# Optimization experiments

Measured on AMD Instinct MI355X. Metric: run time of the kernel, lower is better.

Reference implementation:

```python
import jax, jax.numpy as jnp
import numpy as np

DIM = 2048
N_HEADS = 32
N_KV_HEADS = 8
HEAD_DIM = DIM // N_HEADS  # 64
N_REP = N_HEADS // N_KV_HEADS  # 4
B, S = 1, 2048


def _rope(t, cos, sin):
    # t: (b, s, h, head_dim); cos/sin: (s, head_dim//2)
    tr = t.reshape(*t.shape[:-1], -1, 2)
    a, b = tr[..., 0], tr[..., 1]
    c = cos[None, :, None, :]
    s_ = sin[None, :, None, :]
    ra = a * c - b * s_
    rb = a * s_ + b * c
    return jnp.stack([ra, rb], axis=-1).reshape(t.shape)


def setup_inputs() -> dict:
    key = jax.random.key(0)
    ks = jax.random.split(key, 6)
    sc = 1.0 / np.sqrt(DIM)
    x = jax.random.normal(ks[0], (B, S, DIM), dtype=jnp.float32)
    wq = jax.random.normal(ks[1], (DIM, N_HEADS * HEAD_DIM), dtype=jnp.float32) * sc
    wk = jax.random.normal(ks[2], (DIM, N_KV_HEADS * HEAD_DIM), dtype=jnp.float32) * sc
    wv = jax.random.normal(ks[3], (DIM, N_KV_HEADS * HEAD_DIM), dtype=jnp.float32) * sc
    wo = jax.random.normal(ks[4], (N_HEADS * HEAD_DIM, DIM), dtype=jnp.float32) * sc
    # rotary frequencies (theta = 500000 as in Llama3)
    inv = 1.0 / (500000.0 ** (np.arange(0, HEAD_DIM, 2, dtype=np.float32) / HEAD_DIM))
    ang = np.arange(S, dtype=np.float32)[:, None] * inv[None, :]
    freqs_cos = jnp.asarray(np.cos(ang), dtype=jnp.float32)
    freqs_sin = jnp.asarray(np.sin(ang), dtype=jnp.float32)
    # causal additive mask
    mask = jnp.triu(jnp.full((S, S), -1e9, dtype=jnp.float32), k=1)
    return {"x": x, "wq": wq, "wk": wk, "wv": wv, "wo": wo,
            "freqs_cos": freqs_cos, "freqs_sin": freqs_sin, "mask": mask,
            "start_pos": 0}


def reference(x, wq, wk, wv, wo, freqs_cos, freqs_sin, mask, start_pos):
    b, s, _ = x.shape
    xq = (x @ wq).reshape(b, s, N_HEADS, HEAD_DIM)
    xk = (x @ wk).reshape(b, s, N_KV_HEADS, HEAD_DIM)
    xv = (x @ wv).reshape(b, s, N_KV_HEADS, HEAD_DIM)
    xq = _rope(xq, freqs_cos, freqs_sin)
    xk = _rope(xk, freqs_cos, freqs_sin)
    # GQA without repeat_interleave: view queries as (b, s, kv, rep, d)
    q = xq.reshape(b, s, N_KV_HEADS, N_REP, HEAD_DIM)
    scale = 1.0 / np.sqrt(HEAD_DIM)
    # scores: (b, kv, rep, q, k)
    scores = jnp.einsum('bqkrd,bskd->bkrqs', q, xk) * scale
    scores = scores + mask[None, None, None, :, :]
    probs = jax.nn.softmax(scores.astype(jnp.float32), axis=-1).astype(x.dtype)
    out = jnp.einsum('bkrqs,bskd->bqkrd', probs, xv)
    out = out.reshape(b, s, N_HEADS * HEAD_DIM)
    return out @ wo
```

## Files before the change

kernel.cpp:

```cpp
#include <hip/hip_runtime.h>
#include <hip/hip_bf16.h>

#define DIM 2048
#define S_LEN 2048
#define N_HEADS 32
#define N_KV_HEADS 8
#define HEAD_DIM 64
#define KV_DIM (N_KV_HEADS * HEAD_DIM)
#define QKV_N (DIM + 2 * KV_DIM)
#define QSCALE 0.18033688011112042f

typedef __attribute__((ext_vector_type(8))) short bf16x8;
typedef __attribute__((ext_vector_type(4))) float f32x4;

__device__ __forceinline__ unsigned short bf16_of(float f) {
    __hip_bfloat16 h = __float2bfloat16(f);
    return *reinterpret_cast<unsigned short*>(&h);
}
__device__ __forceinline__ float f_of_bf16(unsigned short u) {
    unsigned int x = ((unsigned int)u) << 16;
    return __uint_as_float(x);
}
__device__ __forceinline__ void gl_lds16(const void* g, void* l) {
    __builtin_amdgcn_global_load_lds((const __attribute__((address_space(1))) void*)g,
                                     (__attribute__((address_space(3))) void*)l, 16, 0, 0);
}
__device__ __forceinline__ unsigned int pack2tr(float lo, float hi) {
    return __builtin_amdgcn_perm(__float_as_uint(hi), __float_as_uint(lo), 0x07060302u);
}

__global__ __launch_bounds__(256) void prep(const float* __restrict__ x,
                                            const float* __restrict__ wq,
                                            const float* __restrict__ wk,
                                            const float* __restrict__ wv,
                                            const float* __restrict__ wo,
                                            unsigned short* __restrict__ xbf,
                                            unsigned short* __restrict__ wqkvT,
                                            unsigned short* __restrict__ woT) {
    __shared__ float tile[64][65];
    const int t = threadIdx.x;
    int b = blockIdx.x;
    if (b < 4096) {
        int idx = b * 256 + t;
        float4 f = ((const float4*)x)[idx];
        ushort4 u;
        u.x = bf16_of(f.x); u.y = bf16_of(f.y); u.z = bf16_of(f.z); u.w = bf16_of(f.w);
        ((ushort4*)xbf)[idx] = u;
        return;
    }
    b -= 4096;
    const float* src;
    unsigned short* dst;
    int src_cols, bx, by;
    if (b < 1024)      { src = wq; dst = wqkvT;                                src_cols = DIM;    bx = b & 31;          by = b >> 5; }
    else if (b < 1280) { src = wk; dst = wqkvT + (size_t)DIM * DIM;            src_cols = KV_DIM; bx = (b - 1024) & 7;  by = (b - 1024) >> 3; }
    else if (b < 1536) { src = wv; dst = wqkvT + (size_t)(DIM + KV_DIM) * DIM; src_cols = KV_DIM; bx = (b - 1280) & 7;  by = (b - 1280) >> 3; }
    else               { src = wo; dst = woT;                                  src_cols = DIM;    bx = (b - 1536) & 31; by = (b - 1536) >> 5; }
    const int c0 = bx * 64, r0 = by * 64;
#pragma unroll
    for (int i = 0; i < 16; i++) {
        int idx = t + i * 256;
        int r = idx >> 6, c = idx & 63;
        tile[r][c] = src[(size_t)(r0 + r) * src_cols + c0 + c];
    }
    __syncthreads();
#pragma unroll
    for (int i = 0; i < 16; i++) {
        int idx = t + i * 256;
        int r = idx >> 6, c = idx & 63;
        dst[(size_t)(c0 + r) * DIM + r0 + c] = bf16_of(tile[c][r]);
    }
}

__global__ __launch_bounds__(256) void gemm_bt64(const unsigned short* __restrict__ A,
                                                 const unsigned short* __restrict__ Bt,
                                                 void* __restrict__ Cv,
                                                 int M, int N, int K, int c_bf16) {
    __shared__ unsigned short As[128 * 64];
    __shared__ unsigned short Bs[64 * 64];
    const int tid = threadIdx.x;
    const int wave = tid >> 6, lane = tid & 63;
    const int m16 = lane & 15, quad = lane >> 4;
    const int m0 = blockIdx.y * 128, n0 = blockIdx.x * 64;
    const int wm = (wave >> 1) * 64, wn = (wave & 1) * 32;

    const int lrow = lane >> 3;
    const int gc = (lane & 7) ^ lrow;
    const unsigned short* Ab = A + (size_t)(m0 + wave * 8 + lrow) * K + gc * 8;
    const unsigned short* Bb = Bt + (size_t)(n0 + wave * 8 + lrow) * K + gc * 8;

    f32x4 acc[4][2];
#pragma unroll
    for (int mb = 0; mb < 4; mb++)
#pragma unroll
        for (int nb = 0; nb < 2; nb++) acc[mb][nb] = (f32x4){0.f, 0.f, 0.f, 0.f};

    for (int k0 = 0; k0 < K; k0 += 64) {
#pragma unroll
        for (int g = 0; g < 4; g++)
            gl_lds16(Ab + (size_t)g * 32 * K + k0, &As[(g * 32 + wave * 8) * 64]);
#pragma unroll
        for (int g = 0; g < 2; g++)
            gl_lds16(Bb + (size_t)g * 32 * K + k0, &Bs[(g * 32 + wave * 8) * 64]);
        __syncthreads();
#pragma unroll
        for (int ks = 0; ks < 2; ks++) {
            const int ch = (ks * 4 + quad) ^ (m16 & 7);
            bf16x8 af[4], bfr[2];
#pragma unroll
            for (int mb = 0; mb < 4; mb++)
                af[mb] = *(const bf16x8*)&As[(wm + mb * 16 + m16) * 64 + ch * 8];
#pragma unroll
            for (int nb = 0; nb < 2; nb++)
                bfr[nb] = *(const bf16x8*)&Bs[(wn + nb * 16 + m16) * 64 + ch * 8];
#pragma unroll
            for (int mb = 0; mb < 4; mb++)
#pragma unroll
                for (int nb = 0; nb < 2; nb++)
                    acc[mb][nb] = __builtin_amdgcn_mfma_f32_16x16x32_bf16(af[mb], bfr[nb], acc[mb][nb], 0, 0, 0);
        }
        __syncthreads();
    }

    if (c_bf16) {
        unsigned short* C = (unsigned short*)Cv;
#pragma unroll
        for (int mb = 0; mb < 4; mb++)
#pragma unroll
            for (int nb = 0; nb < 2; nb++)
#pragma unroll
                for (int r = 0; r < 4; r++)
                    C[(size_t)(m0 + wm + mb * 16 + quad * 4 + r) * N + n0 + wn + nb * 16 + m16] =
                        bf16_of(acc[mb][nb][r]);
    } else {
        float* C = (float*)Cv;
#pragma unroll
        for (int mb = 0; mb < 4; mb++)
#pragma unroll
            for (int nb = 0; nb < 2; nb++)
#pragma unroll
                for (int r = 0; r < 4; r++)
                    C[(size_t)(m0 + wm + mb * 16 + quad * 4 + r) * N + n0 + wn + nb * 16 + m16] =
                        acc[mb][nb][r];
    }
}

__global__ __launch_bounds__(256) void rope_tv(const unsigned short* __restrict__ qkv,
                                               unsigned short* __restrict__ qbf,
                                               unsigned short* __restrict__ kbf,
                                               unsigned short* __restrict__ vbt,
                                               const float* __restrict__ fcos,
                                               const float* __restrict__ fsin) {
    __shared__ unsigned short tile[64][65];
    const int t = threadIdx.x;
    int b = blockIdx.x;
    if (b < 2560) {
        int idx = b * 256 + t;
        const int nq = S_LEN * N_HEADS * 8;
        int s, j, srcoff, dstoff;
        unsigned short* dst;
        float osc;
        if (idx < nq) {
            s = idx >> 8;
            int rem = idx & 255;
            int h = rem >> 3;
            j = rem & 7;
            srcoff = s * QKV_N + h * 64 + j * 8;
            dstoff = s * DIM + h * 64 + j * 8;
            dst = qbf;
            osc = QSCALE;
        } else {
            int t2 = idx - nq;
            s = t2 >> 6;
            int rem = t2 & 63;
            int h = rem >> 3;
            j = rem & 7;
            srcoff = s * QKV_N + DIM + h * 64 + j * 8;
            dstoff = s * KV_DIM + h * 64 + j * 8;
            dst = kbf;
            osc = 1.0f;
        }
        bf16x8 v8 = *(const bf16x8*)&qkv[srcoff];
        float4 c4 = *(const float4*)&fcos[s * 32 + j * 4];
        float4 s4 = *(const float4*)&fsin[s * 32 + j * 4];
        float cs[4] = {c4.x, c4.y, c4.z, c4.w};
        float sn[4] = {s4.x, s4.y, s4.z, s4.w};
        bf16x8 o;
#pragma unroll
        for (int p = 0; p < 4; p++) {
            float a = f_of_bf16((unsigned short)v8[2 * p]);
            float bb = f_of_bf16((unsigned short)v8[2 * p + 1]);
            o[2 * p]     = (short)bf16_of((a * cs[p] - bb * sn[p]) * osc);
            o[2 * p + 1] = (short)bf16_of((a * sn[p] + bb * cs[p]) * osc);
        }
        *(bf16x8*)&dst[dstoff] = o;
        return;
    }
    b -= 2560;
    const int d0 = (b & 7) * 64;
    const int s0 = (b >> 3) * 64;
#pragma unroll
    for (int i = 0; i < 16; i++) {
        int idx = t + i * 256;
        int r = idx >> 6, c = idx & 63;
        tile[r][c] = qkv[(size_t)(s0 + r) * QKV_N + DIM + KV_DIM + d0 + c];
    }
    __syncthreads();
#pragma unroll
    for (int i = 0; i < 16; i++) {
        int idx = t + i * 256;
        int r = idx >> 6, c = idx & 63;
        int key = s0 + c;
        int kl = key & 127;
        int kp = (kl & 0x60) | ((kl & 0x0C) << 1) | ((kl & 0x10) >> 2) | (kl & 3);
        vbt[(size_t)(d0 + r) * S_LEN + (key & ~127) + kp] = tile[c][r];
    }
}

__global__ __launch_bounds__(256) void attn_mfma5(const unsigned short* __restrict__ qb,
                                                  const unsigned short* __restrict__ kb,
                                                  const unsigned short* __restrict__ vbt,
                                                  unsigned short* __restrict__ out) {
    const int h  = blockIdx.y;
    const int bx = blockIdx.x;
    const int kh = h >> 2;
    const int tid  = threadIdx.x;
    const int wave = tid >> 6;
    const int lane = tid & 63;
    const int m16  = lane & 15;
    const int quad = lane >> 4;

    __shared__ unsigned short Ks[2][128 * 64];
    __shared__ unsigned short Vt[2][64 * 128];

    const int lrow8 = lane >> 3;
    const int kc    = (lane & 7) ^ lrow8;
    const int lrow4 = lane >> 4;
    const int vc    = (lane & 15) ^ ((wave * 4 + lrow4) & 7);

    const unsigned short* Kbase = kb + (size_t)kh * 64 + (size_t)(wave * 8 + lrow8) * KV_DIM + kc * 8;
    const unsigned short* Vbase = vbt + (size_t)(kh * 64 + wave * 4 + lrow4) * S_LEN + vc * 8;

    bf16x8 ones;
#pragma unroll
    for (int i = 0; i < 8; i++) ones[i] = (short)0x3F80;

#pragma unroll
    for (int half = 0; half < 2; half++) {
        const int qt = half ? bx : (31 - bx);
        const int q0 = qt * 64;
        const int n_iter = (qt >> 1) + 1;

        bf16x8 qa[2];
        {
            const int qrow = q0 + wave * 16 + m16;
#pragma unroll
            for (int ks = 0; ks < 2; ks++)
                qa[ks] = *(const bf16x8*)&qb[(size_t)qrow * DIM + h * 64 + ks * 32 + quad * 8];
        }

        f32x4 o_acc[4];
#pragma unroll
        for (int nb = 0; nb < 4; nb++) o_acc[nb] = (f32x4){0.f, 0.f, 0.f, 0.f};
        f32x4 l_acc = (f32x4){0.f, 0.f, 0.f, 0.f};
        float m_s = -1e30f;
        const int qrow_lane = q0 + wave * 16 + m16;
        const int orow_base = q0 + wave * 16 + quad * 4;

        if (half) __syncthreads();

#pragma unroll
        for (int g = 0; g < 4; g++) {
            gl_lds16(Kbase + (size_t)(g * 32) * KV_DIM, &Ks[0][(g * 32 + wave * 8) * 64]);
            gl_lds16(Vbase + (size_t)g * 16 * S_LEN, &Vt[0][(g * 16 + wave * 4) * 128]);
        }

        for (int kt = 0; kt < n_iter; kt++) {
            __syncthreads();
            if (kt + 1 < n_iter) {
                const int nb2 = (kt + 1) & 1;
#pragma unroll
                for (int g = 0; g < 4; g++) {
                    gl_lds16(Kbase + (size_t)((kt + 1) * 128 + g * 32) * KV_DIM,
                             &Ks[nb2][(g * 32 + wave * 8) * 64]);
                    gl_lds16(Vbase + (size_t)g * 16 * S_LEN + (kt + 1) * 128,
                             &Vt[nb2][(g * 16 + wave * 4) * 128]);
                }
            }
            const unsigned short* K_ = Ks[kt & 1];
            const unsigned short* V_ = Vt[kt & 1];

            f32x4 sc[8];
#pragma unroll
            for (int cb = 0; cb < 8; cb++) sc[cb] = (f32x4){0.f, 0.f, 0.f, 0.f};
#pragma unroll
            for (int ks = 0; ks < 2; ks++) {
                const int slot = (ks * 4 + quad) ^ (m16 & 7);
#pragma unroll
                for (int cb = 0; cb < 8; cb++) {
                    bf16x8 kf = *(const bf16x8*)&K_[(cb * 16 + m16) * 64 + slot * 8];
                    sc[cb] = __builtin_amdgcn_mfma_f32_16x16x32_bf16(kf, qa[ks], sc[cb], 0, 0, 0);
                }
            }

            if (kt == n_iter - 1) {
#pragma unroll
                for (int cb = 0; cb < 8; cb++) {
                    int key = kt * 128 + cb * 16 + quad * 4;
#pragma unroll
                    for (int r = 0; r < 4; r++)
                        if (key + r > qrow_lane) sc[cb][r] = -1e30f;
                }
            }

            float rmax = fmaxf(fmaxf(sc[0][0], sc[0][1]), fmaxf(sc[0][2], sc[0][3]));
#pragma unroll
            for (int cb = 1; cb < 8; cb++) {
                float c1 = fmaxf(fmaxf(sc[cb][0], sc[cb][1]), fmaxf(sc[cb][2], sc[cb][3]));
                rmax = fmaxf(rmax, c1);
            }
            rmax = fmaxf(rmax, __shfl_xor(rmax, 16, 64));
            rmax = fmaxf(rmax, __shfl_xor(rmax, 32, 64));

            float mnew = fmaxf(m_s, rmax);
            float alpha = __builtin_amdgcn_exp2f(m_s - mnew);
            m_s = mnew;

#pragma unroll
            for (int cb = 0; cb < 8; cb++)
#pragma unroll
                for (int r = 0; r < 4; r++)
                    sc[cb][r] = __builtin_amdgcn_exp2f(sc[cb][r] - mnew);

            unsigned int P01[8], P23[8];
#pragma unroll
            for (int cb = 0; cb < 8; cb++) {
                P01[cb] = pack2tr(sc[cb][0], sc[cb][1]);
                P23[cb] = pack2tr(sc[cb][2], sc[cb][3]);
            }

#pragma unroll
            for (int r = 0; r < 4; r++) {
                float a_r = __shfl(alpha, quad * 4 + r, 64);
#pragma unroll
                for (int nb = 0; nb < 4; nb++) o_acc[nb][r] *= a_r;
                l_acc[r] *= a_r;
            }

#pragma unroll
            for (int ks = 0; ks < 4; ks++) {
                union { unsigned int u[4]; bf16x8 v; } pa;
                pa.u[0] = P01[2 * ks];     pa.u[1] = P23[2 * ks];
                pa.u[2] = P01[2 * ks + 1]; pa.u[3] = P23[2 * ks + 1];
                const int slot = (ks * 4 + quad) ^ (m16 & 7);
#pragma unroll
                for (int nb = 0; nb < 4; nb++) {
                    bf16x8 vf = *(const bf16x8*)&V_[(nb * 16 + m16) * 128 + slot * 8];
                    o_acc[nb] = __builtin_amdgcn_mfma_f32_16x16x32_bf16(pa.v, vf, o_acc[nb], 0, 0, 0);
                }
                l_acc = __builtin_amdgcn_mfma_f32_16x16x32_bf16(pa.v, ones, l_acc, 0, 0, 0);
            }
        }

#pragma unroll
        for (int r = 0; r < 4; r++) {
            float inv_l = 1.f / l_acc[r];
#pragma unroll
            for (int nb = 0; nb < 4; nb++)
                out[(size_t)(orow_base + r) * DIM + h * 64 + nb * 16 + m16] =
                    bf16_of(o_acc[nb][r] * inv_l);
        }
    }
}

extern "C" void kernel_launch(void* const* d_in, const int* in_sizes, int n_in,
                              void* d_out, int out_size, void* d_ws, size_t ws_size,
                              hipStream_t stream) {
    const float* x    = (const float*)d_in[0];
    const float* wq   = (const float*)d_in[1];
    const float* wk   = (const float*)d_in[2];
    const float* wv   = (const float*)d_in[3];
    const float* wo   = (const float*)d_in[4];
    const float* fcos = (const float*)d_in[5];
    const float* fsin = (const float*)d_in[6];

    char* ws = (char*)d_ws;
    const size_t MB = 1024 * 1024;
    unsigned short* xbf    = (unsigned short*)(ws);
    unsigned short* wqkvT  = (unsigned short*)(ws + 8 * MB);
    unsigned short* woT    = (unsigned short*)(ws + 20 * MB);
    unsigned short* qkvbf  = (unsigned short*)(ws + 28 * MB);
    unsigned short* vbt    = (unsigned short*)(ws + 40 * MB);
    unsigned short* qbf    = (unsigned short*)(ws + 8 * MB);
    unsigned short* kbf    = (unsigned short*)(ws + 16 * MB);
    unsigned short* attnbf = (unsigned short*)(ws);

    prep<<<4096 + 2560, 256, 0, stream>>>(x, wq, wk, wv, wo, xbf, wqkvT, woT);

    gemm_bt64<<<dim3(QKV_N / 64, S_LEN / 128), 256, 0, stream>>>(xbf, wqkvT, qkvbf,
                                                                 S_LEN, QKV_N, DIM, 1);

    rope_tv<<<2560 + 256, 256, 0, stream>>>(qkvbf, qbf, kbf, vbt, fcos, fsin);

    attn_mfma5<<<dim3(16, N_HEADS), 256, 0, stream>>>(qbf, kbf, vbt, attnbf);

    gemm_bt64<<<dim3(DIM / 64, S_LEN / 128), 256, 0, stream>>>(attnbf, woT, d_out,
                                                               S_LEN, DIM, DIM, 0);
}
```

Measured before the change: 227.7 us.

## Process 128-row query tiles per block, sharing K/V loads across two sub-tiles

The attention kernel no longer processes two balanced 64-row query tiles one after the other. Each block now handles one 128-row query tile, and each wave keeps two 16-row sub-tiles (A and B) in registers. Every K fragment and V fragment read from LDS feeds two MFMAs, which halves K/V global-to-LDS traffic per query row and doubles the independent MFMA chains. In exchange, register use goes up and the old pairing that balanced causal work across blocks is gone. The new code relies on launching heavy tiles first to keep per-block work even.

Measured after the change: 242.4 us. +6.5%, slower.

```diff
diff --git a/kernel.cpp b/kernel.cpp
--- a/kernel.cpp
+++ b/kernel.cpp
@@ -217,12 +217,14 @@
     }
 }
 
-__global__ __launch_bounds__(256) void attn_mfma5(const unsigned short* __restrict__ qb,
+__global__ __launch_bounds__(256) void attn_mfma6(const unsigned short* __restrict__ qb,
                                                   const unsigned short* __restrict__ kb,
                                                   const unsigned short* __restrict__ vbt,
                                                   unsigned short* __restrict__ out) {
     const int h  = blockIdx.y;
-    const int bx = blockIdx.x;
+    const int qt = 15 - blockIdx.x;
+    const int q0 = qt * 128;
+    const int n_iter = qt + 1;
     const int kh = h >> 2;
     const int tid  = threadIdx.x;
     const int wave = tid >> 6;
@@ -245,130 +247,143 @@
 #pragma unroll
     for (int i = 0; i < 8; i++) ones[i] = (short)0x3F80;
 
-#pragma unroll
-    for (int half = 0; half < 2; half++) {
-        const int qt = half ? bx : (31 - bx);
-        const int q0 = qt * 64;
-        const int n_iter = (qt >> 1) + 1;
-
-        bf16x8 qa[2];
-        {
-            const int qrow = q0 + wave * 16 + m16;
-#pragma unroll
-            for (int ks = 0; ks < 2; ks++)
-                qa[ks] = *(const bf16x8*)&qb[(size_t)qrow * DIM + h * 64 + ks * 32 + quad * 8];
-        }
-
-        f32x4 o_acc[4];
-#pragma unroll
-        for (int nb = 0; nb < 4; nb++) o_acc[nb] = (f32x4){0.f, 0.f, 0.f, 0.f};
-        f32x4 l_acc = (f32x4){0.f, 0.f, 0.f, 0.f};
-        float m_s = -1e30f;
-        const int qrow_lane = q0 + wave * 16 + m16;
-        const int orow_base = q0 + wave * 16 + quad * 4;
-
-        if (half) __syncthreads();
-
-#pragma unroll
-        for (int g = 0; g < 4; g++) {
-            gl_lds16(Kbase + (size_t)(g * 32) * KV_DIM, &Ks[0][(g * 32 + wave * 8) * 64]);
-            gl_lds16(Vbase + (size_t)g * 16 * S_LEN, &Vt[0][(g * 16 + wave * 4) * 128]);
-        }
-
-        for (int kt = 0; kt < n_iter; kt++) {
-            __syncthreads();
-            if (kt + 1 < n_iter) {
-                const int nb2 = (kt + 1) & 1;
-#pragma unroll
-                for (int g = 0; g < 4; g++) {
-                    gl_lds16(Kbase + (size_t)((kt + 1) * 128 + g * 32) * KV_DIM,
-                             &Ks[nb2][(g * 32 + wave * 8) * 64]);
-                    gl_lds16(Vbase + (size_t)g * 16 * S_LEN + (kt + 1) * 128,
-                             &Vt[nb2][(g * 16 + wave * 4) * 128]);
+    const int rowA = q0 + wave * 16 + m16;
+    const int rowB = rowA + 64;
+    bf16x8 qaA[2], qaB[2];
+#pragma unroll
+    for (int ks = 0; ks < 2; ks++) {
+        qaA[ks] = *(const bf16x8*)&qb[(size_t)rowA * DIM + h * 64 + ks * 32 + quad * 8];
+        qaB[ks] = *(const bf16x8*)&qb[(size_t)rowB * DIM + h * 64 + ks * 32 + quad * 8];
+    }
+
+    f32x4 oA[4], oB[4];
+#pragma unroll
+    for (int nb = 0; nb < 4; nb++) {
+        oA[nb] = (f32x4){0.f, 0.f, 0.f, 0.f};
+        oB[nb] = (f32x4){0.f, 0.f, 0.f, 0.f};
+    }
+    f32x4 lA = (f32x4){0.f, 0.f, 0.f, 0.f};
+    f32x4 lB = (f32x4){0.f, 0.f, 0.f, 0.f};
+    float mA = -1e30f, mB = -1e30f;
+
+#pragma unroll
+    for (int g = 0; g < 4; g++) {
+        gl_lds16(Kbase + (size_t)(g * 32) * KV_DIM, &Ks[0][(g * 32 + wave * 8) * 64]);
+        gl_lds16(Vbase + (size_t)g * 16 * S_LEN, &Vt[0][(g * 16 + wave * 4) * 128]);
+    }
+
+    for (int kt = 0; kt < n_iter; kt++) {
+        __syncthreads();
+        if (kt + 1 < n_iter) {
+            const int nb2 = (kt + 1) & 1;
+#pragma unroll
+            for (int g = 0; g < 4; g++) {
+                gl_lds16(Kbase + (size_t)((kt + 1) * 128 + g * 32) * KV_DIM,
+                         &Ks[nb2][(g * 32 + wave * 8) * 64]);
+                gl_lds16(Vbase + (size_t)g * 16 * S_LEN + (kt + 1) * 128,
+                         &Vt[nb2][(g * 16 + wave * 4) * 128]);
+            }
+        }
+        const unsigned short* K_ = Ks[kt & 1];
+        const unsigned short* V_ = Vt[kt & 1];
+
+        f32x4 sa[8], sb[8];
+#pragma unroll
+        for (int cb = 0; cb < 8; cb++) {
+            sa[cb] = (f32x4){0.f, 0.f, 0.f, 0.f};
+            sb[cb] = (f32x4){0.f, 0.f, 0.f, 0.f};
+        }
+#pragma unroll
+        for (int ks = 0; ks < 2; ks++) {
+            const int slot = (ks * 4 + quad) ^ (m16 & 7);
+#pragma unroll
+            for (int cb = 0; cb < 8; cb++) {
+                bf16x8 kf = *(const bf16x8*)&K_[(cb * 16 + m16) * 64 + slot * 8];
+                sa[cb] = __builtin_amdgcn_mfma_f32_16x16x32_bf16(kf, qaA[ks], sa[cb], 0, 0, 0);
+                sb[cb] = __builtin_amdgcn_mfma_f32_16x16x32_bf16(kf, qaB[ks], sb[cb], 0, 0, 0);
+            }
+        }
+
+        if (kt == n_iter - 1) {
+#pragma unroll
+            for (int cb = 0; cb < 8; cb++) {
+                int key = kt * 128 + cb * 16 + quad * 4;
+#pragma unroll
+                for (int r = 0; r < 4; r++) {
+                    if (key + r > rowA) sa[cb][r] = -1e30f;
+                    if (key + r > rowB) sb[cb][r] = -1e30f;
                 }
             }
-            const unsigned short* K_ = Ks[kt & 1];
-            const unsigned short* V_ = Vt[kt & 1];
-
-            f32x4 sc[8];
-#pragma unroll
-            for (int cb = 0; cb < 8; cb++) sc[cb] = (f32x4){0.f, 0.f, 0.f, 0.f};
-#pragma unroll
-            for (int ks = 0; ks < 2; ks++) {
-                const int slot = (ks * 4 + quad) ^ (m16 & 7);
-#pragma unroll
-                for (int cb = 0; cb < 8; cb++) {
-                    bf16x8 kf = *(const bf16x8*)&K_[(cb * 16 + m16) * 64 + slot * 8];
-                    sc[cb] = __builtin_amdgcn_mfma_f32_16x16x32_bf16(kf, qa[ks], sc[cb], 0, 0, 0);
-                }
+        }
+
+        float rmaxA = fmaxf(fmaxf(sa[0][0], sa[0][1]), fmaxf(sa[0][2], sa[0][3]));
+        float rmaxB = fmaxf(fmaxf(sb[0][0], sb[0][1]), fmaxf(sb[0][2], sb[0][3]));
+#pragma unroll
+        for (int cb = 1; cb < 8; cb++) {
+            rmaxA = fmaxf(rmaxA, fmaxf(fmaxf(sa[cb][0], sa[cb][1]), fmaxf(sa[cb][2], sa[cb][3])));
+            rmaxB = fmaxf(rmaxB, fmaxf(fmaxf(sb[cb][0], sb[cb][1]), fmaxf(sb[cb][2], sb[cb][3])));
+        }
+        rmaxA = fmaxf(rmaxA, __shfl_xor(rmaxA, 16, 64));
+        rmaxB = fmaxf(rmaxB, __shfl_xor(rmaxB, 16, 64));
+        rmaxA = fmaxf(rmaxA, __shfl_xor(rmaxA, 32, 64));
+        rmaxB = fmaxf(rmaxB, __shfl_xor(rmaxB, 32, 64));
+
+        float mnA = fmaxf(mA, rmaxA);
+        float mnB = fmaxf(mB, rmaxB);
+        float alA = __builtin_amdgcn_exp2f(mA - mnA);
+        float alB = __builtin_amdgcn_exp2f(mB - mnB);
+        mA = mnA; mB = mnB;
+
+#pragma unroll
+        for (int cb = 0; cb < 8; cb++)
+#pragma unroll
+            for (int r = 0; r < 4; r++) {
+                sa[cb][r] = __builtin_amdgcn_exp2f(sa[cb][r] - mnA);
+                sb[cb][r] = __builtin_amdgcn_exp2f(sb[cb][r] - mnB);
             }
 
-            if (kt == n_iter - 1) {
-#pragma unroll
-                for (int cb = 0; cb < 8; cb++) {
-                    int key = kt * 128 + cb * 16 + quad * 4;
-#pragma unroll
-                    for (int r = 0; r < 4; r++)
-                        if (key + r > qrow_lane) sc[cb][r] = -1e30f;
-                }
+#pragma unroll
+        for (int r = 0; r < 4; r++) {
+            float aAr = __shfl(alA, quad * 4 + r, 64);
+            float aBr = __shfl(alB, quad * 4 + r, 64);
+#pragma unroll
+            for (int nb = 0; nb < 4; nb++) { oA[nb][r] *= aAr; oB[nb][r] *= aBr; }
+            lA[r] *= aAr; lB[r] *= aBr;
+        }
+
+#pragma unroll
+        for (int ks = 0; ks < 4; ks++) {
+            union { unsigned int u[4]; bf16x8 v; } pA, pB;
+            pA.u[0] = pack2tr(sa[2 * ks][0], sa[2 * ks][1]);
+            pA.u[1] = pack2tr(sa[2 * ks][2], sa[2 * ks][3]);
+            pA.u[2] = pack2tr(sa[2 * ks + 1][0], sa[2 * ks + 1][1]);
+            pA.u[3] = pack2tr(sa[2 * ks + 1][2], sa[2 * ks + 1][3]);
+            pB.u[0] = pack2tr(sb[2 * ks][0], sb[2 * ks][1]);
+            pB.u[1] = pack2tr(sb[2 * ks][2], sb[2 * ks][3]);
+            pB.u[2] = pack2tr(sb[2 * ks + 1][0], sb[2 * ks + 1][1]);
+            pB.u[3] = pack2tr(sb[2 * ks + 1][2], sb[2 * ks + 1][3]);
+            const int slot = (ks * 4 + quad) ^ (m16 & 7);
+#pragma unroll
+            for (int nb = 0; nb < 4; nb++) {
+                bf16x8 vf = *(const bf16x8*)&V_[(nb * 16 + m16) * 128 + slot * 8];
+                oA[nb] = __builtin_amdgcn_mfma_f32_16x16x32_bf16(pA.v, vf, oA[nb], 0, 0, 0);
+                oB[nb] = __builtin_amdgcn_mfma_f32_16x16x32_bf16(pB.v, vf, oB[nb], 0, 0, 0);
             }
-
-            float rmax = fmaxf(fmaxf(sc[0][0], sc[0][1]), fmaxf(sc[0][2], sc[0][3]));
-#pragma unroll
-            for (int cb = 1; cb < 8; cb++) {
-                float c1 = fmaxf(fmaxf(sc[cb][0], sc[cb][1]), fmaxf(sc[cb][2], sc[cb][3]));
-                rmax = fmaxf(rmax, c1);
-            }
-            rmax = fmaxf(rmax, __shfl_xor(rmax, 16, 64));
-            rmax = fmaxf(rmax, __shfl_xor(rmax, 32, 64));
-
-            float mnew = fmaxf(m_s, rmax);
-            float alpha = __builtin_amdgcn_exp2f(m_s - mnew);
-            m_s = mnew;
-
-#pragma unroll
-            for (int cb = 0; cb < 8; cb++)
-#pragma unroll
-                for (int r = 0; r < 4; r++)
-                    sc[cb][r] = __builtin_amdgcn_exp2f(sc[cb][r] - mnew);
-
-            unsigned int P01[8], P23[8];
-#pragma unroll
-            for (int cb = 0; cb < 8; cb++) {
-                P01[cb] = pack2tr(sc[cb][0], sc[cb][1]);
-                P23[cb] = pack2tr(sc[cb][2], sc[cb][3]);
-            }
-
-#pragma unroll
-            for (int r = 0; r < 4; r++) {
-                float a_r = __shfl(alpha, quad * 4 + r, 64);
-#pragma unroll
-                for (int nb = 0; nb < 4; nb++) o_acc[nb][r] *= a_r;
-                l_acc[r] *= a_r;
-            }
-
-#pragma unroll
-            for (int ks = 0; ks < 4; ks++) {
-                union { unsigned int u[4]; bf16x8 v; } pa;
-                pa.u[0] = P01[2 * ks];     pa.u[1] = P23[2 * ks];
-                pa.u[2] = P01[2 * ks + 1]; pa.u[3] = P23[2 * ks + 1];
-                const int slot = (ks * 4 + quad) ^ (m16 & 7);
-#pragma unroll
-                for (int nb = 0; nb < 4; nb++) {
-                    bf16x8 vf = *(const bf16x8*)&V_[(nb * 16 + m16) * 128 + slot * 8];
-                    o_acc[nb] = __builtin_amdgcn_mfma_f32_16x16x32_bf16(pa.v, vf, o_acc[nb], 0, 0, 0);
-                }
-                l_acc = __builtin_amdgcn_mfma_f32_16x16x32_bf16(pa.v, ones, l_acc, 0, 0, 0);
-            }
-        }
-
-#pragma unroll
-        for (int r = 0; r < 4; r++) {
-            float inv_l = 1.f / l_acc[r];
-#pragma unroll
-            for (int nb = 0; nb < 4; nb++)
-                out[(size_t)(orow_base + r) * DIM + h * 64 + nb * 16 + m16] =
-                    bf16_of(o_acc[nb][r] * inv_l);
+            lA = __builtin_amdgcn_mfma_f32_16x16x32_bf16(pA.v, ones, lA, 0, 0, 0);
+            lB = __builtin_amdgcn_mfma_f32_16x16x32_bf16(pB.v, ones, lB, 0, 0, 0);
+        }
+    }
+
+    const int orowA = q0 + wave * 16 + quad * 4;
+    const int orowB = orowA + 64;
+#pragma unroll
+    for (int r = 0; r < 4; r++) {
+        float invA = 1.f / lA[r];
+        float invB = 1.f / lB[r];
+#pragma unroll
+        for (int nb = 0; nb < 4; nb++) {
+            out[(size_t)(orowA + r) * DIM + h * 64 + nb * 16 + m16] = bf16_of(oA[nb][r] * invA);
+            out[(size_t)(orowB + r) * DIM + h * 64 + nb * 16 + m16] = bf16_of(oB[nb][r] * invB);
         }
     }
 }
@@ -402,7 +417,7 @@
 
     rope_tv<<<2560 + 256, 256, 0, stream>>>(qkvbf, qbf, kbf, vbt, fcos, fsin);
 
-    attn_mfma5<<<dim3(16, N_HEADS), 256, 0, stream>>>(qbf, kbf, vbt, attnbf);
+    attn_mfma6<<<dim3(16, N_HEADS), 256, 0, stream>>>(qbf, kbf, vbt, attnbf);
 
     gemm_bt64<<<dim3(DIM / 64, S_LEN / 128), 256, 0, stream>>>(attnbf, woT, d_out,
                                                                S_LEN, DIM, DIM, 0);
```

## Double-buffer GEMM LDS loads and widen tile to 128x128

Applied to the files above, without the earlier changes.

The GEMM kernel now uses a 128x128 output tile in place of 128x64, and double-buffers the A and B shared-memory tiles. The next K-slice is loaded while the current one is consumed, so one barrier per iteration is removed. This is meant to raise MFMA work per LDS load and hide global-to-LDS latency. In exchange it uses more LDS (64KB) and more accumulator registers, and halves the grid (e.g. 256 blocks for the output projection), which may hurt occupancy and CU fill on a 256-CU part.

Measured after the change: 233.8 us. 1.03x slower.

```diff
diff --git a/kernel.cpp b/kernel.cpp
--- a/kernel.cpp
+++ b/kernel.cpp
@@ -72,54 +72,65 @@
     }
 }
 
-__global__ __launch_bounds__(256) void gemm_bt64(const unsigned short* __restrict__ A,
-                                                 const unsigned short* __restrict__ Bt,
-                                                 void* __restrict__ Cv,
-                                                 int M, int N, int K, int c_bf16) {
-    __shared__ unsigned short As[128 * 64];
-    __shared__ unsigned short Bs[64 * 64];
+__global__ __launch_bounds__(256) void gemm_bt128(const unsigned short* __restrict__ A,
+                                                  const unsigned short* __restrict__ Bt,
+                                                  void* __restrict__ Cv,
+                                                  int M, int N, int K, int c_bf16) {
+    __shared__ unsigned short As[2][128 * 64];
+    __shared__ unsigned short Bs[2][128 * 64];
     const int tid = threadIdx.x;
     const int wave = tid >> 6, lane = tid & 63;
     const int m16 = lane & 15, quad = lane >> 4;
-    const int m0 = blockIdx.y * 128, n0 = blockIdx.x * 64;
-    const int wm = (wave >> 1) * 64, wn = (wave & 1) * 32;
+    const int m0 = blockIdx.y * 128, n0 = blockIdx.x * 128;
+    const int wm = (wave >> 1) * 64, wn = (wave & 1) * 64;
 
     const int lrow = lane >> 3;
     const int gc = (lane & 7) ^ lrow;
     const unsigned short* Ab = A + (size_t)(m0 + wave * 8 + lrow) * K + gc * 8;
     const unsigned short* Bb = Bt + (size_t)(n0 + wave * 8 + lrow) * K + gc * 8;
 
-    f32x4 acc[4][2];
+    f32x4 acc[4][4];
 #pragma unroll
     for (int mb = 0; mb < 4; mb++)
 #pragma unroll
-        for (int nb = 0; nb < 2; nb++) acc[mb][nb] = (f32x4){0.f, 0.f, 0.f, 0.f};
-
-    for (int k0 = 0; k0 < K; k0 += 64) {
-#pragma unroll
-        for (int g = 0; g < 4; g++)
-            gl_lds16(Ab + (size_t)g * 32 * K + k0, &As[(g * 32 + wave * 8) * 64]);
-#pragma unroll
-        for (int g = 0; g < 2; g++)
-            gl_lds16(Bb + (size_t)g * 32 * K + k0, &Bs[(g * 32 + wave * 8) * 64]);
+        for (int nb = 0; nb < 4; nb++) acc[mb][nb] = (f32x4){0.f, 0.f, 0.f, 0.f};
+
+    const int n_steps = K >> 6;
+
+#pragma unroll
+    for (int g = 0; g < 4; g++) {
+        gl_lds16(Ab + (size_t)g * 32 * K, &As[0][(g * 32 + wave * 8) * 64]);
+        gl_lds16(Bb + (size_t)g * 32 * K, &Bs[0][(g * 32 + wave * 8) * 64]);
+    }
+
+    for (int i = 0; i < n_steps; i++) {
         __syncthreads();
+        if (i + 1 < n_steps) {
+            const int nb2 = (i + 1) & 1;
+            const int k0 = (i + 1) << 6;
+#pragma unroll
+            for (int g = 0; g < 4; g++) {
+                gl_lds16(Ab + (size_t)g * 32 * K + k0, &As[nb2][(g * 32 + wave * 8) * 64]);
+                gl_lds16(Bb + (size_t)g * 32 * K + k0, &Bs[nb2][(g * 32 + wave * 8) * 64]);
+            }
+        }
+        const unsigned short* A_ = As[i & 1];
+        const unsigned short* B_ = Bs[i & 1];
 #pragma unroll
         for (int ks = 0; ks < 2; ks++) {
             const int ch = (ks * 4 + quad) ^ (m16 & 7);
-            bf16x8 af[4], bfr[2];
+            bf16x8 af[4], bfr[4];
+#pragma unroll
+            for (int mb = 0; mb < 4; mb++) {
+                af[mb]  = *(const bf16x8*)&A_[(wm + mb * 16 + m16) * 64 + ch * 8];
+                bfr[mb] = *(const bf16x8*)&B_[(wn + mb * 16 + m16) * 64 + ch * 8];
+            }
 #pragma unroll
             for (int mb = 0; mb < 4; mb++)
-                af[mb] = *(const bf16x8*)&As[(wm + mb * 16 + m16) * 64 + ch * 8];
-#pragma unroll
-            for (int nb = 0; nb < 2; nb++)
-                bfr[nb] = *(const bf16x8*)&Bs[(wn + nb * 16 + m16) * 64 + ch * 8];
-#pragma unroll
-            for (int mb = 0; mb < 4; mb++)
-#pragma unroll
-                for (int nb = 0; nb < 2; nb++)
+#pragma unroll
+                for (int nb = 0; nb < 4; nb++)
                     acc[mb][nb] = __builtin_amdgcn_mfma_f32_16x16x32_bf16(af[mb], bfr[nb], acc[mb][nb], 0, 0, 0);
         }
-        __syncthreads();
     }
 
     if (c_bf16) {
@@ -127,7 +138,7 @@
 #pragma unroll
         for (int mb = 0; mb < 4; mb++)
 #pragma unroll
-            for (int nb = 0; nb < 2; nb++)
+            for (int nb = 0; nb < 4; nb++)
 #pragma unroll
                 for (int r = 0; r < 4; r++)
                     C[(size_t)(m0 + wm + mb * 16 + quad * 4 + r) * N + n0 + wn + nb * 16 + m16] =
@@ -137,7 +148,7 @@
 #pragma unroll
         for (int mb = 0; mb < 4; mb++)
 #pragma unroll
-            for (int nb = 0; nb < 2; nb++)
+            for (int nb = 0; nb < 4; nb++)
 #pragma unroll
                 for (int r = 0; r < 4; r++)
                     C[(size_t)(m0 + wm + mb * 16 + quad * 4 + r) * N + n0 + wn + nb * 16 + m16] =
@@ -397,13 +408,13 @@
 
     prep<<<4096 + 2560, 256, 0, stream>>>(x, wq, wk, wv, wo, xbf, wqkvT, woT);
 
-    gemm_bt64<<<dim3(QKV_N / 64, S_LEN / 128), 256, 0, stream>>>(xbf, wqkvT, qkvbf,
-                                                                 S_LEN, QKV_N, DIM, 1);
+    gemm_bt128<<<dim3(QKV_N / 128, S_LEN / 128), 256, 0, stream>>>(xbf, wqkvT, qkvbf,
+                                                                   S_LEN, QKV_N, DIM, 1);
 
     rope_tv<<<2560 + 256, 256, 0, stream>>>(qkvbf, qbf, kbf, vbt, fcos, fsin);
 
     attn_mfma5<<<dim3(16, N_HEADS), 256, 0, stream>>>(qbf, kbf, vbt, attnbf);
 
-    gemm_bt64<<<dim3(DIM / 64, S_LEN / 128), 256, 0, stream>>>(attnbf, woT, d_out,
-                                                               S_LEN, DIM, DIM, 0);
-}
+    gemm_bt128<<<dim3(DIM / 128, S_LEN / 128), 256, 0, stream>>>(attnbf, woT, d_out,
+                                                                 S_LEN, DIM, DIM, 0);
+}
```

## Fuse RoPE into QKV GEMM epilogue and double-buffer GEMM LDS tiles

Applied to the files above, without the earlier changes.

The QKV projection GEMM now applies rotary embedding and query scaling directly in its epilogue, using a lane shuffle to pair even/odd columns, and writes Q, K, V to separate buffers. This removes the standalone rope pass and its extra round trip through global memory, leaving only a small V transpose kernel. Both GEMMs also switch to double-buffered LDS with prefetch of the next K tile, which doubles shared memory per block and may lower occupancy.

After: 231.1 us. About the same (+1.5%).

```diff
diff --git a/kernel.cpp b/kernel.cpp
--- a/kernel.cpp
+++ b/kernel.cpp
@@ -72,17 +72,21 @@
     }
 }
 
-__global__ __launch_bounds__(256) void gemm_bt64(const unsigned short* __restrict__ A,
-                                                 const unsigned short* __restrict__ Bt,
-                                                 void* __restrict__ Cv,
-                                                 int M, int N, int K, int c_bf16) {
-    __shared__ unsigned short As[128 * 64];
-    __shared__ unsigned short Bs[64 * 64];
+__global__ __launch_bounds__(256) void gemm_qkv(const unsigned short* __restrict__ A,
+                                                const unsigned short* __restrict__ Bt,
+                                                unsigned short* __restrict__ qbf,
+                                                unsigned short* __restrict__ kbf,
+                                                unsigned short* __restrict__ vbf,
+                                                const float* __restrict__ fcos,
+                                                const float* __restrict__ fsin) {
+    __shared__ unsigned short As[2][128 * 64];
+    __shared__ unsigned short Bs[2][64 * 64];
     const int tid = threadIdx.x;
     const int wave = tid >> 6, lane = tid & 63;
     const int m16 = lane & 15, quad = lane >> 4;
     const int m0 = blockIdx.y * 128, n0 = blockIdx.x * 64;
     const int wm = (wave >> 1) * 64, wn = (wave & 1) * 32;
+    const int K = DIM;
 
     const int lrow = lane >> 3;
     const int gc = (lane & 7) ^ lrow;
@@ -95,31 +99,144 @@
 #pragma unroll
         for (int nb = 0; nb < 2; nb++) acc[mb][nb] = (f32x4){0.f, 0.f, 0.f, 0.f};
 
-    for (int k0 = 0; k0 < K; k0 += 64) {
-#pragma unroll
-        for (int g = 0; g < 4; g++)
-            gl_lds16(Ab + (size_t)g * 32 * K + k0, &As[(g * 32 + wave * 8) * 64]);
-#pragma unroll
-        for (int g = 0; g < 2; g++)
-            gl_lds16(Bb + (size_t)g * 32 * K + k0, &Bs[(g * 32 + wave * 8) * 64]);
+#pragma unroll
+    for (int g = 0; g < 4; g++)
+        gl_lds16(Ab + (size_t)g * 32 * K, &As[0][(g * 32 + wave * 8) * 64]);
+#pragma unroll
+    for (int g = 0; g < 2; g++)
+        gl_lds16(Bb + (size_t)g * 32 * K, &Bs[0][(g * 32 + wave * 8) * 64]);
+
+    const int n_steps = K >> 6;
+    for (int i = 0; i < n_steps; i++) {
         __syncthreads();
+        if (i + 1 < n_steps) {
+            const int nb2 = (i + 1) & 1;
+            const int k0 = (i + 1) << 6;
+#pragma unroll
+            for (int g = 0; g < 4; g++)
+                gl_lds16(Ab + (size_t)g * 32 * K + k0, &As[nb2][(g * 32 + wave * 8) * 64]);
+#pragma unroll
+            for (int g = 0; g < 2; g++)
+                gl_lds16(Bb + (size_t)g * 32 * K + k0, &Bs[nb2][(g * 32 + wave * 8) * 64]);
+        }
+        const unsigned short* A_ = As[i & 1];
+        const unsigned short* B_ = Bs[i & 1];
 #pragma unroll
         for (int ks = 0; ks < 2; ks++) {
             const int ch = (ks * 4 + quad) ^ (m16 & 7);
             bf16x8 af[4], bfr[2];
 #pragma unroll
             for (int mb = 0; mb < 4; mb++)
-                af[mb] = *(const bf16x8*)&As[(wm + mb * 16 + m16) * 64 + ch * 8];
+                af[mb] = *(const bf16x8*)&A_[(wm + mb * 16 + m16) * 64 + ch * 8];
 #pragma unroll
             for (int nb = 0; nb < 2; nb++)
-                bfr[nb] = *(const bf16x8*)&Bs[(wn + nb * 16 + m16) * 64 + ch * 8];
+                bfr[nb] = *(const bf16x8*)&B_[(wn + nb * 16 + m16) * 64 + ch * 8];
 #pragma unroll
             for (int mb = 0; mb < 4; mb++)
 #pragma unroll
                 for (int nb = 0; nb < 2; nb++)
                     acc[mb][nb] = __builtin_amdgcn_mfma_f32_16x16x32_bf16(af[mb], bfr[nb], acc[mb][nb], 0, 0, 0);
         }
+    }
+
+    if (n0 >= DIM + KV_DIM) {
+#pragma unroll
+        for (int mb = 0; mb < 4; mb++)
+#pragma unroll
+            for (int nb = 0; nb < 2; nb++)
+#pragma unroll
+                for (int r = 0; r < 4; r++)
+                    vbf[(size_t)(m0 + wm + mb * 16 + quad * 4 + r) * KV_DIM +
+                        (n0 - DIM - KV_DIM) + wn + nb * 16 + m16] = bf16_of(acc[mb][nb][r]);
+        return;
+    }
+    const bool is_q = (n0 < DIM);
+    const float osc = is_q ? QSCALE : 1.0f;
+    unsigned short* dst = is_q ? qbf : kbf;
+    const int dst_stride = is_q ? DIM : KV_DIM;
+    const int cbase = is_q ? n0 : (n0 - DIM);
+    const int odd = m16 & 1;
+#pragma unroll
+    for (int nb = 0; nb < 2; nb++) {
+        const int col = cbase + wn + nb * 16 + m16;
+        const int fi = (col >> 1) & 31;
+#pragma unroll
+        for (int mb = 0; mb < 4; mb++) {
+#pragma unroll
+            for (int r = 0; r < 4; r++) {
+                const int s = m0 + wm + mb * 16 + quad * 4 + r;
+                float v = acc[mb][nb][r];
+                float p = __shfl_xor(v, 1, 64);
+                float c = fcos[s * 32 + fi] * osc;
+                float sn = fsin[s * 32 + fi] * osc;
+                float o = odd ? (p * sn + v * c) : (v * c - p * sn);
+                dst[(size_t)s * dst_stride + col] = bf16_of(o);
+            }
+        }
+    }
+}
+
+__global__ __launch_bounds__(256) void gemm_bt64d(const unsigned short* __restrict__ A,
+                                                  const unsigned short* __restrict__ Bt,
+                                                  void* __restrict__ Cv,
+                                                  int M, int N, int K, int c_bf16) {
+    __shared__ unsigned short As[2][128 * 64];
+    __shared__ unsigned short Bs[2][64 * 64];
+    const int tid = threadIdx.x;
+    const int wave = tid >> 6, lane = tid & 63;
+    const int m16 = lane & 15, quad = lane >> 4;
+    const int m0 = blockIdx.y * 128, n0 = blockIdx.x * 64;
+    const int wm = (wave >> 1) * 64, wn = (wave & 1) * 32;
+
+    const int lrow = lane >> 3;
+    const int gc = (lane & 7) ^ lrow;
+    const unsigned short* Ab = A + (size_t)(m0 + wave * 8 + lrow) * K + gc * 8;
+    const unsigned short* Bb = Bt + (size_t)(n0 + wave * 8 + lrow) * K + gc * 8;
+
+    f32x4 acc[4][2];
+#pragma unroll
+    for (int mb = 0; mb < 4; mb++)
+#pragma unroll
+        for (int nb = 0; nb < 2; nb++) acc[mb][nb] = (f32x4){0.f, 0.f, 0.f, 0.f};
+
+#pragma unroll
+    for (int g = 0; g < 4; g++)
+        gl_lds16(Ab + (size_t)g * 32 * K, &As[0][(g * 32 + wave * 8) * 64]);
+#pragma unroll
+    for (int g = 0; g < 2; g++)
+        gl_lds16(Bb + (size_t)g * 32 * K, &Bs[0][(g * 32 + wave * 8) * 64]);
+
+    const int n_steps = K >> 6;
+    for (int i = 0; i < n_steps; i++) {
         __syncthreads();
+        if (i + 1 < n_steps) {
+            const int nb2 = (i + 1) & 1;
+            const int k0 = (i + 1) << 6;
+#pragma unroll
+            for (int g = 0; g < 4; g++)
+                gl_lds16(Ab + (size_t)g * 32 * K + k0, &As[nb2][(g * 32 + wave * 8) * 64]);
+#pragma unroll
+            for (int g = 0; g < 2; g++)
+                gl_lds16(Bb + (size_t)g * 32 * K + k0, &Bs[nb2][(g * 32 + wave * 8) * 64]);
+        }
+        const unsigned short* A_ = As[i & 1];
+        const unsigned short* B_ = Bs[i & 1];
+#pragma unroll
+        for (int ks = 0; ks < 2; ks++) {
+            const int ch = (ks * 4 + quad) ^ (m16 & 7);
+            bf16x8 af[4], bfr[2];
+#pragma unroll
+            for (int mb = 0; mb < 4; mb++)
+                af[mb] = *(const bf16x8*)&A_[(wm + mb * 16 + m16) * 64 + ch * 8];
+#pragma unroll
+            for (int nb = 0; nb < 2; nb++)
+                bfr[nb] = *(const bf16x8*)&B_[(wn + nb * 16 + m16) * 64 + ch * 8];
+#pragma unroll
+            for (int mb = 0; mb < 4; mb++)
+#pragma unroll
+                for (int nb = 0; nb < 2; nb++)
+                    acc[mb][nb] = __builtin_amdgcn_mfma_f32_16x16x32_bf16(af[mb], bfr[nb], acc[mb][nb], 0, 0, 0);
+        }
     }
 
     if (c_bf16) {
@@ -145,65 +262,17 @@
     }
 }
 
-__global__ __launch_bounds__(256) void rope_tv(const unsigned short* __restrict__ qkv,
-                                               unsigned short* __restrict__ qbf,
-                                               unsigned short* __restrict__ kbf,
-                                               unsigned short* __restrict__ vbt,
-                                               const float* __restrict__ fcos,
-                                               const float* __restrict__ fsin) {
+__global__ __launch_bounds__(256) void transpose_v(const unsigned short* __restrict__ vbf,
+                                                   unsigned short* __restrict__ vbt) {
     __shared__ unsigned short tile[64][65];
     const int t = threadIdx.x;
-    int b = blockIdx.x;
-    if (b < 2560) {
-        int idx = b * 256 + t;
-        const int nq = S_LEN * N_HEADS * 8;
-        int s, j, srcoff, dstoff;
-        unsigned short* dst;
-        float osc;
-        if (idx < nq) {
-            s = idx >> 8;
-            int rem = idx & 255;
-            int h = rem >> 3;
-            j = rem & 7;
-            srcoff = s * QKV_N + h * 64 + j * 8;
-            dstoff = s * DIM + h * 64 + j * 8;
-            dst = qbf;
-            osc = QSCALE;
-        } else {
-            int t2 = idx - nq;
-            s = t2 >> 6;
-            int rem = t2 & 63;
-            int h = rem >> 3;
-            j = rem & 7;
-            srcoff = s * QKV_N + DIM + h * 64 + j * 8;
-            dstoff = s * KV_DIM + h * 64 + j * 8;
-            dst = kbf;
-            osc = 1.0f;
-        }
-        bf16x8 v8 = *(const bf16x8*)&qkv[srcoff];
-        float4 c4 = *(const float4*)&fcos[s * 32 + j * 4];
-        float4 s4 = *(const float4*)&fsin[s * 32 + j * 4];
-        float cs[4] = {c4.x, c4.y, c4.z, c4.w};
-        float sn[4] = {s4.x, s4.y, s4.z, s4.w};
-        bf16x8 o;
-#pragma unroll
-        for (int p = 0; p < 4; p++) {
-            float a = f_of_bf16((unsigned short)v8[2 * p]);
-            float bb = f_of_bf16((unsigned short)v8[2 * p + 1]);
-            o[2 * p]     = (short)bf16_of((a * cs[p] - bb * sn[p]) * osc);
-            o[2 * p + 1] = (short)bf16_of((a * sn[p] + bb * cs[p]) * osc);
-        }
-        *(bf16x8*)&dst[dstoff] = o;
-        return;
-    }
-    b -= 2560;
-    const int d0 = (b & 7) * 64;
-    const int s0 = (b >> 3) * 64;
+    const int d0 = blockIdx.x * 64;
+    const int s0 = blockIdx.y * 64;
 #pragma unroll
     for (int i = 0; i < 16; i++) {
         int idx = t + i * 256;
         int r = idx >> 6, c = idx & 63;
-        tile[r][c] = qkv[(size_t)(s0 + r) * QKV_N + DIM + KV_DIM + d0 + c];
+        tile[r][c] = vbf[(size_t)(s0 + r) * KV_DIM + d0 + c];
     }
     __syncthreads();
 #pragma unroll
@@ -389,21 +458,21 @@
     unsigned short* xbf    = (unsigned short*)(ws);
     unsigned short* wqkvT  = (unsigned short*)(ws + 8 * MB);
     unsigned short* woT    = (unsigned short*)(ws + 20 * MB);
-    unsigned short* qkvbf  = (unsigned short*)(ws + 28 * MB);
+    unsigned short* qbf    = (unsigned short*)(ws + 28 * MB);
+    unsigned short* kbf    = (unsigned short*)(ws + 36 * MB);
+    unsigned short* vbf    = (unsigned short*)(ws + 38 * MB);
     unsigned short* vbt    = (unsigned short*)(ws + 40 * MB);
-    unsigned short* qbf    = (unsigned short*)(ws + 8 * MB);
-    unsigned short* kbf    = (unsigned short*)(ws + 16 * MB);
     unsigned short* attnbf = (unsigned short*)(ws);
 
     prep<<<4096 + 2560, 256, 0, stream>>>(x, wq, wk, wv, wo, xbf, wqkvT, woT);
 
-    gemm_bt64<<<dim3(QKV_N / 64, S_LEN / 128), 256, 0, stream>>>(xbf, wqkvT, qkvbf,
-                                                                 S_LEN, QKV_N, DIM, 1);
-
-    rope_tv<<<2560 + 256, 256, 0, stream>>>(qkvbf, qbf, kbf, vbt, fcos, fsin);
+    gemm_qkv<<<dim3(QKV_N / 64, S_LEN / 128), 256, 0, stream>>>(xbf, wqkvT,
+                                                                qbf, kbf, vbf, fcos, fsin);
+
+    transpose_v<<<dim3(KV_DIM / 64, S_LEN / 64), 256, 0, stream>>>(vbf, vbt);
 
     attn_mfma5<<<dim3(16, N_HEADS), 256, 0, stream>>>(qbf, kbf, vbt, attnbf);
 
-    gemm_bt64<<<dim3(DIM / 64, S_LEN / 128), 256, 0, stream>>>(attnbf, woT, d_out,
-                                                               S_LEN, DIM, DIM, 0);
-}
+    gemm_bt64d<<<dim3(DIM / 64, S_LEN / 128), 256, 0, stream>>>(attnbf, woT, d_out,
+                                                                S_LEN, DIM, DIM, 0);
+}
```
